# Kernel tuning notes

Hardware: AMD Instinct MI355X
Metric: run time of the kernel (lower is better)

## Reference

```python
import jax, jax.numpy as jnp
import numpy as np

LUT_DIM = 33
CTX_DIM = 128


def _identity_lut(dim):
    coords = jnp.linspace(0.0, 1.0, dim)
    r, g, b = jnp.meshgrid(coords, coords, coords, indexing='ij')
    return jnp.stack([r, g, b], axis=-1)  # [dim, dim, dim, 3], axes (r,g,b)


def setup_inputs() -> dict:
    key = jax.random.key(0)
    ks = jax.random.split(key, 8)
    B, H, W = 4, 512, 512
    image = jax.random.normal(ks[0], (B, 3, H, W), dtype=jnp.float32)
    spatial_context = jax.random.normal(ks[1], (B, CTX_DIM, H, W), dtype=jnp.float32)
    s = 0.05
    params = {
        'base_lut': _identity_lut(LUT_DIM),
        'W1': jax.random.normal(ks[2], (128, CTX_DIM), dtype=jnp.float32) * s,
        'b1': jnp.zeros((128,), dtype=jnp.float32),
        'W2': jax.random.normal(ks[3], (64, 128), dtype=jnp.float32) * s,
        'b2': jnp.zeros((64,), dtype=jnp.float32),
        'W3': jax.random.normal(ks[4], (3, 64), dtype=jnp.float32) * s,
        'b3': jnp.zeros((3,), dtype=jnp.float32),
        'offset_scale': jnp.float32(0.1),
    }
    return {'image': image, 'spatial_context': spatial_context, **params}


def _conv1x1(x, W, b):
    # x: [B,Cin,H,W], W: [Cout,Cin]
    return jnp.einsum('bchw,oc->bohw', x, W) + b[None, :, None, None]


def _trilinear_lut(lut_flat, gx, gy, gz, dim):
    # lut_flat: [3, dim^3] (flattened over z,y,x = r,g,b axes)
    # gx,gy,gz: [B,H,W] float coords in [0, dim-1]; border padding via clamp
    fmax = jnp.float32(dim - 1)
    gx = jnp.clip(gx, 0.0, fmax)
    gy = jnp.clip(gy, 0.0, fmax)
    gz = jnp.clip(gz, 0.0, fmax)
    x0 = jnp.floor(gx).astype(jnp.int32)
    y0 = jnp.floor(gy).astype(jnp.int32)
    z0 = jnp.floor(gz).astype(jnp.int32)
    x1 = jnp.minimum(x0 + 1, dim - 1)
    y1 = jnp.minimum(y0 + 1, dim - 1)
    z1 = jnp.minimum(z0 + 1, dim - 1)
    fx = gx - x0.astype(gx.dtype)
    fy = gy - y0.astype(gy.dtype)
    fz = gz - z0.astype(gz.dtype)

    def gather(zi, yi, xi):
        idx = (zi * dim + yi) * dim + xi  # [B,H,W]
        return lut_flat[:, idx]  # [3,B,H,W]

    c000 = gather(z0, y0, x0); c001 = gather(z0, y0, x1)
    c010 = gather(z0, y1, x0); c011 = gather(z0, y1, x1)
    c100 = gather(z1, y0, x0); c101 = gather(z1, y0, x1)
    c110 = gather(z1, y1, x0); c111 = gather(z1, y1, x1)

    fx = fx[None]; fy = fy[None]; fz = fz[None]
    c00 = c000 * (1 - fx) + c001 * fx
    c01 = c010 * (1 - fx) + c011 * fx
    c10 = c100 * (1 - fx) + c101 * fx
    c11 = c110 * (1 - fx) + c111 * fx
    c0 = c00 * (1 - fy) + c01 * fy
    c1 = c10 * (1 - fy) + c11 * fy
    out = c0 * (1 - fz) + c1 * fz  # [3,B,H,W]
    return jnp.transpose(out, (1, 0, 2, 3))  # [B,3,H,W]


def reference(image, spatial_context, base_lut, W1, b1, W2, b2, W3, b3, offset_scale):
    dim = base_lut.shape[0]
    gelu = lambda v: jax.nn.gelu(v, approximate=False)
    h = gelu(_conv1x1(spatial_context, W1, b1))
    h = gelu(_conv1x1(h, W2, b2))
    offset = jnp.tanh(_conv1x1(h, W3, b3)) * offset_scale  # [B,3,H,W]

    img01 = jnp.clip((image + 1.0) * 0.5, 0.0, 1.0)
    # grid_sample convention: grid channel0 (R)->x->last LUT axis (b),
    # channel1 (G)->y->g axis, channel2 (B)->z->r axis; align_corners=True.
    scale = jnp.float32(dim - 1)
    gx = img01[:, 0] * scale  # R -> b axis
    gy = img01[:, 1] * scale  # G -> g axis
    gz = img01[:, 2] * scale  # B -> r axis
    # base_lut [r,g,b,3] -> channels-first [3, r(=z), g(=y), b(=x)] -> flatten
    lut_flat = jnp.transpose(base_lut, (3, 0, 1, 2)).reshape(3, dim * dim * dim)
    sampled = _trilinear_lut(lut_flat, gx, gy, gz, dim)  # [B,3,H,W]
    return sampled * 2.0 - 1.0 + offset
```

## Files before the change

### kernel.cpp

```cpp
#include <hip/hip_runtime.h>
#include <stdint.h>

#define HW 262144
#define LDIM 33

typedef __bf16 bf16x8 __attribute__((ext_vector_type(8)));
typedef float  f32x4  __attribute__((ext_vector_type(4)));

union BF8 { bf16x8 v; unsigned u[4]; };

__device__ __forceinline__ unsigned bfr1(float a) {
  unsigned u = __float_as_uint(a);
  return (u + 0x7fffu + ((u >> 16) & 1u)) >> 16;
}
__device__ __forceinline__ unsigned pk2(float a, float b) {
  return bfr1(a) | (bfr1(b) << 16);
}
__device__ __forceinline__ float tanh_fast(float x) {
  return 1.0f - 2.0f / (__expf(2.0f * x) + 1.0f);
}
__device__ __forceinline__ float gelu_t(float x) {
  float t = tanh_fast(0.7978845608028654f * (x + 0.044715f * x * x * x));
  return 0.5f * x * (1.0f + t);
}

__global__ __launch_bounds__(256, 2) void local3dlut_kernel(
    const float* __restrict__ img,  const float* __restrict__ ctx,
    const float* __restrict__ lut,  const float* __restrict__ W1,
    const float* __restrict__ b1,   const float* __restrict__ W2,
    const float* __restrict__ b2,   const float* __restrict__ W3,
    const float* __restrict__ b3,   const float* __restrict__ oscp,
    float* __restrict__ out)
{
  __shared__ uint4 smem4[4096];
  char* sm = (char*)smem4;
  const int t    = threadIdx.x;
  const int lane = t & 63;
  const int wv   = t >> 6;
  const int n    = lane & 15;
  const int q    = lane >> 4;

  #pragma unroll
  for (int rep = 0; rep < 16; ++rep) {
    int f4 = t + 256 * rep;
    float4 v = ((const float4*)W1)[f4];
    int fi = f4 << 2;
    int o = fi >> 7, k = fi & 127;
    char* dst = sm + o * 256 + (((k >> 3) ^ (o & 15)) << 4) + ((k & 7) << 1);
    *(uint2*)dst = make_uint2(pk2(v.x, v.y), pk2(v.z, v.w));
  }
  #pragma unroll
  for (int rep = 0; rep < 8; ++rep) {
    int f4 = t + 256 * rep;
    float4 v = ((const float4*)W2)[f4];
    int fi = f4 << 2;
    int o = fi >> 7, k = fi & 127;
    char* dst = sm + 32768 + o * 256 + (((k >> 3) ^ (o & 15)) << 4) + ((k & 7) << 1);
    *(uint2*)dst = make_uint2(pk2(v.x, v.y), pk2(v.z, v.w));
  }
  __syncthreads();

  float b1r[8], b2r[4], w3r[3][4];
  #pragma unroll
  for (int i = 0; i < 8; ++i) b1r[i] = b1[i * 16 + n];
  #pragma unroll
  for (int i = 0; i < 4; ++i) b2r[i] = b2[i * 16 + n];
  #pragma unroll
  for (int j = 0; j < 3; ++j)
    #pragma unroll
    for (int i = 0; i < 4; ++i) w3r[j][i] = W3[j * 64 + i * 16 + n];
  const float b3r0 = b3[0], b3r1 = b3[1], b3r2 = b3[2];
  const float osc  = oscp[0];

  const int p0   = blockIdx.x * 512;
  const int bi   = p0 >> 18;
  const int sblk = p0 & (HW - 1);
  const float* ctxB = ctx + (size_t)bi * ((size_t)128 * HW);
  const float* imgB = img + (size_t)bi * ((size_t)3 * HW);
  float*       outB = out + (size_t)bi * ((size_t)3 * HW);
  char* hb = sm + 49152 + wv * 4096;

  #pragma unroll 1
  for (int it = 0; it < 4; ++it) {
    const int sw = sblk + it * 128 + wv * 32;

    BF8 a1[2][4];
    #pragma unroll
    for (int mt = 0; mt < 2; ++mt) {
      const int sA = sw + mt * 16 + n;
      #pragma unroll
      for (int ks = 0; ks < 4; ++ks) {
        const float* cb = ctxB + (size_t)(ks * 32 + q * 8) * HW + sA;
        float v0 = cb[0];
        float v1 = cb[(size_t)1 * HW];
        float v2 = cb[(size_t)2 * HW];
        float v3 = cb[(size_t)3 * HW];
        float v4 = cb[(size_t)4 * HW];
        float v5 = cb[(size_t)5 * HW];
        float v6 = cb[(size_t)6 * HW];
        float v7 = cb[(size_t)7 * HW];
        a1[mt][ks].u[0] = pk2(v0, v1);
        a1[mt][ks].u[1] = pk2(v2, v3);
        a1[mt][ks].u[2] = pk2(v4, v5);
        a1[mt][ks].u[3] = pk2(v6, v7);
      }
    }

    f32x4 acc2[2][4];
    #pragma unroll
    for (int mt = 0; mt < 2; ++mt)
      #pragma unroll
      for (int j = 0; j < 4; ++j) { f32x4 z = {0.f,0.f,0.f,0.f}; acc2[mt][j] = z; }

    #pragma unroll
    for (int half = 0; half < 2; ++half) {
      f32x4 acc1[2][4];
      #pragma unroll
      for (int mt = 0; mt < 2; ++mt)
        #pragma unroll
        for (int j = 0; j < 4; ++j) { f32x4 z = {0.f,0.f,0.f,0.f}; acc1[mt][j] = z; }

      #pragma unroll
      for (int ks = 0; ks < 4; ++ks) {
        #pragma unroll
        for (int nt4 = 0; nt4 < 4; ++nt4) {
          int row = (half * 4 + nt4) * 16 + n;
          bf16x8 bw = *(const bf16x8*)(sm + row * 256 + ((((ks << 2) + q) ^ n) << 4));
          acc1[0][nt4] = __builtin_amdgcn_mfma_f32_16x16x32_bf16(a1[0][ks].v, bw, acc1[0][nt4], 0, 0, 0);
          acc1[1][nt4] = __builtin_amdgcn_mfma_f32_16x16x32_bf16(a1[1][ks].v, bw, acc1[1][nt4], 0, 0, 0);
        }
      }
      #pragma unroll
      for (int mt = 0; mt < 2; ++mt)
        #pragma unroll
        for (int nt4 = 0; nt4 < 4; ++nt4) {
          int fl = nt4 * 16 + n;
          int kgf = fl >> 3;
          #pragma unroll
          for (int r = 0; r < 4; ++r) {
            int px = mt * 16 + (q << 2) + r;
            float hv = gelu_t(acc1[mt][nt4][r] + b1r[half * 4 + nt4]);
            *(unsigned short*)(hb + px * 128 + ((kgf ^ (px & 7)) << 4) + ((fl & 7) << 1)) =
                (unsigned short)bfr1(hv);
          }
        }
      #pragma unroll
      for (int ks2 = 0; ks2 < 2; ++ks2) {
        bf16x8 a2[2];
        #pragma unroll
        for (int mt = 0; mt < 2; ++mt) {
          int px = mt * 16 + n;
          a2[mt] = *(const bf16x8*)(hb + px * 128 + ((((ks2 << 2) + q) ^ (px & 7)) << 4));
        }
        #pragma unroll
        for (int nt2 = 0; nt2 < 4; ++nt2) {
          int row = nt2 * 16 + n;
          int kg2 = half * 8 + (ks2 << 2) + q;
          bf16x8 bw = *(const bf16x8*)(sm + 32768 + row * 256 + ((kg2 ^ n) << 4));
          acc2[0][nt2] = __builtin_amdgcn_mfma_f32_16x16x32_bf16(a2[0], bw, acc2[0][nt2], 0, 0, 0);
          acc2[1][nt2] = __builtin_amdgcn_mfma_f32_16x16x32_bf16(a2[1], bw, acc2[1][nt2], 0, 0, 0);
        }
      }
    }

    #pragma unroll
    for (int mt = 0; mt < 2; ++mt)
      #pragma unroll
      for (int nt2 = 0; nt2 < 4; ++nt2)
        #pragma unroll
        for (int r = 0; r < 4; ++r)
          acc2[mt][nt2][r] = gelu_t(acc2[mt][nt2][r] + b2r[nt2]);

    #pragma unroll
    for (int mt = 0; mt < 2; ++mt)
      #pragma unroll
      for (int r = 0; r < 4; ++r) {
        float h0 = acc2[mt][0][r], h1v = acc2[mt][1][r], h2v = acc2[mt][2][r], h3v = acc2[mt][3][r];
        float pa = w3r[0][0]*h0 + w3r[0][1]*h1v + w3r[0][2]*h2v + w3r[0][3]*h3v;
        float pb = w3r[1][0]*h0 + w3r[1][1]*h1v + w3r[1][2]*h2v + w3r[1][3]*h3v;
        float pc = w3r[2][0]*h0 + w3r[2][1]*h1v + w3r[2][2]*h2v + w3r[2][3]*h3v;
        pa += __shfl_xor(pa, 1, 16); pa += __shfl_xor(pa, 2, 16);
        pa += __shfl_xor(pa, 4, 16); pa += __shfl_xor(pa, 8, 16);
        pb += __shfl_xor(pb, 1, 16); pb += __shfl_xor(pb, 2, 16);
        pb += __shfl_xor(pb, 4, 16); pb += __shfl_xor(pb, 8, 16);
        pc += __shfl_xor(pc, 1, 16); pc += __shfl_xor(pc, 2, 16);
        pc += __shfl_xor(pc, 4, 16); pc += __shfl_xor(pc, 8, 16);
        int px = mt * 16 + (q << 2) + r;
        float sel  = (n == 0) ? pa   : ((n == 1) ? pb   : pc);
        float bsel = (n == 0) ? b3r0 : ((n == 1) ? b3r1 : b3r2);
        float ov = tanh_fast(sel + bsel) * osc;
        if (n < 3) *(float*)(hb + px * 12 + (n << 2)) = ov;
      }

    if (lane < 32) {
      const int sp = sw + lane;
      float o0 = *(const float*)(hb + lane * 12 + 0);
      float o1 = *(const float*)(hb + lane * 12 + 4);
      float o2 = *(const float*)(hb + lane * 12 + 8);

      float rr = imgB[sp], gg = imgB[HW + sp], bb = imgB[2 * HW + sp];
      float gx = fminf(fmaxf((rr + 1.f) * 0.5f, 0.f), 1.f) * 32.f;
      float gy = fminf(fmaxf((gg + 1.f) * 0.5f, 0.f), 1.f) * 32.f;
      float gz = fminf(fmaxf((bb + 1.f) * 0.5f, 0.f), 1.f) * 32.f;
      int x0 = (int)gx, y0 = (int)gy, z0 = (int)gz;
      float fx = gx - (float)x0, fy = gy - (float)y0, fz = gz - (float)z0;
      int x1 = min(x0 + 1, 32), y1 = min(y0 + 1, 32), z1 = min(z0 + 1, 32);
      int zy00 = (z0 * LDIM + y0) * LDIM, zy01 = (z0 * LDIM + y1) * LDIM;
      int zy10 = (z1 * LDIM + y0) * LDIM, zy11 = (z1 * LDIM + y1) * LDIM;
      int i000 = (zy00 + x0) * 3, i001 = (zy00 + x1) * 3;
      int i010 = (zy01 + x0) * 3, i011 = (zy01 + x1) * 3;
      int i100 = (zy10 + x0) * 3, i101 = (zy10 + x1) * 3;
      int i110 = (zy11 + x0) * 3, i111 = (zy11 + x1) * 3;
      const float* L = lut;
      float so[3];
      #pragma unroll
      for (int ch = 0; ch < 3; ++ch) {
        float c000 = L[i000 + ch], c001 = L[i001 + ch];
        float c010 = L[i010 + ch], c011 = L[i011 + ch];
        float c100 = L[i100 + ch], c101 = L[i101 + ch];
        float c110 = L[i110 + ch], c111 = L[i111 + ch];
        float c00 = c000 + fx * (c001 - c000);
        float c01 = c010 + fx * (c011 - c010);
        float c10 = c100 + fx * (c101 - c100);
        float c11 = c110 + fx * (c111 - c110);
        float ca  = c00 + fy * (c01 - c00);
        float cb2 = c10 + fy * (c11 - c10);
        so[ch] = ca + fz * (cb2 - ca);
      }
      outB[sp]          = so[0] * 2.f - 1.f + o0;
      outB[HW + sp]     = so[1] * 2.f - 1.f + o1;
      outB[2 * HW + sp] = so[2] * 2.f - 1.f + o2;
    }
  }
}

extern "C" void kernel_launch(void* const* d_in, const int* in_sizes, int n_in,
                              void* d_out, int out_size, void* d_ws, size_t ws_size,
                              hipStream_t stream) {
  const float* img = (const float*)d_in[0];
  const float* ctx = (const float*)d_in[1];
  const float* lut = (const float*)d_in[2];
  const float* W1  = (const float*)d_in[3];
  const float* b1  = (const float*)d_in[4];
  const float* W2  = (const float*)d_in[5];
  const float* b2  = (const float*)d_in[6];
  const float* W3  = (const float*)d_in[7];
  const float* b3  = (const float*)d_in[8];
  const float* osc = (const float*)d_in[9];
  float* out = (float*)d_out;
  local3dlut_kernel<<<dim3(2048), dim3(256), 0, stream>>>(
      img, ctx, lut, W1, b1, W2, b2, W3, b3, osc, out);
}
```

Measured before the change: 828.1 us.

## Use 512-thread blocks, hardware bf16 conversion, early image loads, and vectorized LUT gathers

```diff
diff --git a/kernel.cpp b/kernel.cpp
--- a/kernel.cpp
+++ b/kernel.cpp
@@ -5,16 +5,14 @@
 #define LDIM 33
 
 typedef __bf16 bf16x8 __attribute__((ext_vector_type(8)));
+typedef __bf16 bf16x2 __attribute__((ext_vector_type(2)));
 typedef float  f32x4  __attribute__((ext_vector_type(4)));
 
 union BF8 { bf16x8 v; unsigned u[4]; };
 
-__device__ __forceinline__ unsigned bfr1(float a) {
-  unsigned u = __float_as_uint(a);
-  return (u + 0x7fffu + ((u >> 16) & 1u)) >> 16;
-}
 __device__ __forceinline__ unsigned pk2(float a, float b) {
-  return bfr1(a) | (bfr1(b) << 16);
+  bf16x2 p; p[0] = (__bf16)a; p[1] = (__bf16)b;
+  return __builtin_bit_cast(unsigned, p);
 }
 __device__ __forceinline__ float tanh_fast(float x) {
   return 1.0f - 2.0f / (__expf(2.0f * x) + 1.0f);
@@ -24,7 +22,13 @@
   return 0.5f * x * (1.0f + t);
 }
 
-__global__ __launch_bounds__(256, 2) void local3dlut_kernel(
+struct F3 { float x, y, z; };
+__device__ __forceinline__ F3 lerp3(F3 a, F3 b, float f) {
+  F3 r; r.x = a.x + f * (b.x - a.x); r.y = a.y + f * (b.y - a.y);
+  r.z = a.z + f * (b.z - a.z); return r;
+}
+
+__global__ __launch_bounds__(512, 4) void local3dlut_kernel(
     const float* __restrict__ img,  const float* __restrict__ ctx,
     const float* __restrict__ lut,  const float* __restrict__ W1,
     const float* __restrict__ b1,   const float* __restrict__ W2,
@@ -32,7 +36,7 @@
     const float* __restrict__ b3,   const float* __restrict__ oscp,
     float* __restrict__ out)
 {
-  __shared__ uint4 smem4[4096];
+  __shared__ uint4 smem4[5120];
   char* sm = (char*)smem4;
   const int t    = threadIdx.x;
   const int lane = t & 63;
@@ -41,8 +45,8 @@
   const int q    = lane >> 4;
 
   #pragma unroll
-  for (int rep = 0; rep < 16; ++rep) {
-    int f4 = t + 256 * rep;
+  for (int rep = 0; rep < 8; ++rep) {
+    int f4 = t + 512 * rep;
     float4 v = ((const float4*)W1)[f4];
     int fi = f4 << 2;
     int o = fi >> 7, k = fi & 127;
@@ -50,8 +54,8 @@
     *(uint2*)dst = make_uint2(pk2(v.x, v.y), pk2(v.z, v.w));
   }
   #pragma unroll
-  for (int rep = 0; rep < 8; ++rep) {
-    int f4 = t + 256 * rep;
+  for (int rep = 0; rep < 4; ++rep) {
+    int f4 = t + 512 * rep;
     float4 v = ((const float4*)W2)[f4];
     int fi = f4 << 2;
     int o = fi >> 7, k = fi & 127;
@@ -72,7 +76,7 @@
   const float b3r0 = b3[0], b3r1 = b3[1], b3r2 = b3[2];
   const float osc  = oscp[0];
 
-  const int p0   = blockIdx.x * 512;
+  const int p0   = blockIdx.x * 1024;
   const int bi   = p0 >> 18;
   const int sblk = p0 & (HW - 1);
   const float* ctxB = ctx + (size_t)bi * ((size_t)128 * HW);
@@ -82,7 +86,12 @@
 
   #pragma unroll 1
   for (int it = 0; it < 4; ++it) {
-    const int sw = sblk + it * 128 + wv * 32;
+    const int sw = sblk + it * 256 + wv * 32;
+
+    const int spf = sw + (lane & 31);
+    const float rr = imgB[spf];
+    const float gg = imgB[HW + spf];
+    const float bb = imgB[2 * HW + spf];
 
     BF8 a1[2][4];
     #pragma unroll
@@ -140,8 +149,7 @@
           for (int r = 0; r < 4; ++r) {
             int px = mt * 16 + (q << 2) + r;
             float hv = gelu_t(acc1[mt][nt4][r] + b1r[half * 4 + nt4]);
-            *(unsigned short*)(hb + px * 128 + ((kgf ^ (px & 7)) << 4) + ((fl & 7) << 1)) =
-                (unsigned short)bfr1(hv);
+            *(__bf16*)(hb + px * 128 + ((kgf ^ (px & 7)) << 4) + ((fl & 7) << 1)) = (__bf16)hv;
           }
         }
       #pragma unroll
@@ -198,7 +206,6 @@
       float o1 = *(const float*)(hb + lane * 12 + 4);
       float o2 = *(const float*)(hb + lane * 12 + 8);
 
-      float rr = imgB[sp], gg = imgB[HW + sp], bb = imgB[2 * HW + sp];
       float gx = fminf(fmaxf((rr + 1.f) * 0.5f, 0.f), 1.f) * 32.f;
       float gy = fminf(fmaxf((gg + 1.f) * 0.5f, 0.f), 1.f) * 32.f;
       float gz = fminf(fmaxf((bb + 1.f) * 0.5f, 0.f), 1.f) * 32.f;
@@ -207,29 +214,18 @@
       int x1 = min(x0 + 1, 32), y1 = min(y0 + 1, 32), z1 = min(z0 + 1, 32);
       int zy00 = (z0 * LDIM + y0) * LDIM, zy01 = (z0 * LDIM + y1) * LDIM;
       int zy10 = (z1 * LDIM + y0) * LDIM, zy11 = (z1 * LDIM + y1) * LDIM;
-      int i000 = (zy00 + x0) * 3, i001 = (zy00 + x1) * 3;
-      int i010 = (zy01 + x0) * 3, i011 = (zy01 + x1) * 3;
-      int i100 = (zy10 + x0) * 3, i101 = (zy10 + x1) * 3;
-      int i110 = (zy11 + x0) * 3, i111 = (zy11 + x1) * 3;
-      const float* L = lut;
-      float so[3];
-      #pragma unroll
-      for (int ch = 0; ch < 3; ++ch) {
-        float c000 = L[i000 + ch], c001 = L[i001 + ch];
-        float c010 = L[i010 + ch], c011 = L[i011 + ch];
-        float c100 = L[i100 + ch], c101 = L[i101 + ch];
-        float c110 = L[i110 + ch], c111 = L[i111 + ch];
-        float c00 = c000 + fx * (c001 - c000);
-        float c01 = c010 + fx * (c011 - c010);
-        float c10 = c100 + fx * (c101 - c100);
-        float c11 = c110 + fx * (c111 - c110);
-        float ca  = c00 + fy * (c01 - c00);
-        float cb2 = c10 + fy * (c11 - c10);
-        so[ch] = ca + fz * (cb2 - ca);
-      }
-      outB[sp]          = so[0] * 2.f - 1.f + o0;
-      outB[HW + sp]     = so[1] * 2.f - 1.f + o1;
-      outB[2 * HW + sp] = so[2] * 2.f - 1.f + o2;
+      const F3* L3 = (const F3*)lut;
+      F3 c000 = L3[zy00 + x0], c001 = L3[zy00 + x1];
+      F3 c010 = L3[zy01 + x0], c011 = L3[zy01 + x1];
+      F3 c100 = L3[zy10 + x0], c101 = L3[zy10 + x1];
+      F3 c110 = L3[zy11 + x0], c111 = L3[zy11 + x1];
+      F3 c00 = lerp3(c000, c001, fx), c01 = lerp3(c010, c011, fx);
+      F3 c10 = lerp3(c100, c101, fx), c11 = lerp3(c110, c111, fx);
+      F3 ca  = lerp3(c00, c01, fy),   cb2 = lerp3(c10, c11, fy);
+      F3 so  = lerp3(ca, cb2, fz);
+      outB[sp]          = so.x * 2.f - 1.f + o0;
+      outB[HW + sp]     = so.y * 2.f - 1.f + o1;
+      outB[2 * HW + sp] = so.z * 2.f - 1.f + o2;
     }
   }
 }
@@ -248,6 +244,6 @@
   const float* b3  = (const float*)d_in[8];
   const float* osc = (const float*)d_in[9];
   float* out = (float*)d_out;
-  local3dlut_kernel<<<dim3(2048), dim3(256), 0, stream>>>(
+  local3dlut_kernel<<<dim3(1024), dim3(512), 0, stream>>>(
       img, ctx, lut, W1, b1, W2, b2, W3, b3, osc, out);
 }
```

After: 923.2 us. +11.5%, slower.
